# Performance work log

Measured on AMD Instinct MI355X. Metric: run time of the kernel, lower is better.

Reference implementation:

```python
import jax, jax.numpy as jnp
import numpy as np

SCALES = jnp.asarray([0.5, 1.0, 2.0], dtype=jnp.float32)  # distance_scales
GROUP_THRESHOLD = 2.0
EPS = 1e-6


def _pairwise_norm(x):
    # x: (B, T, N, 2) -> (B, T, N, N) euclidean distances, diagonal == 0
    diff = x[:, :, :, None, :] - x[:, :, None, :, :]
    sq = jnp.sum(diff * diff, axis=-1)
    safe = jnp.where(sq > 0, sq, 1.0)
    return jnp.where(sq > 0, jnp.sqrt(safe), 0.0)


def _assign_groups_one(d_last, threshold):
    # d_last: (N, N) pairwise distances at last timestep.
    # Sequential greedy grouping (faithful to the torch loop) via lax.scan over agents.
    N = d_last.shape[0]
    idx = jnp.arange(N)

    def step(carry, i):
        assigned, groups, cur = carry
        is_new = jnp.logical_not(assigned[i])  # agent i starts a new group
        # i itself (dist 0) plus unassigned j > i within threshold
        newly = is_new & jnp.logical_not(assigned) & (d_last[i] <= threshold) & (idx >= i)
        groups = jnp.where(newly, cur, groups)
        assigned = assigned | newly
        cur = cur + is_new.astype(jnp.int32)
        return (assigned, groups, cur), None

    init = (jnp.zeros(N, dtype=bool), jnp.zeros(N, dtype=jnp.int32), jnp.int32(0))
    (_, groups, _), _ = jax.lax.scan(step, init, idx)
    return groups


def setup_inputs() -> dict:
    key = jax.random.key(0)
    k1, k2 = jax.random.split(key)
    B, T, N = 8, 16, 256
    positions = jax.random.uniform(k1, (B, T, N, 2), dtype=jnp.float32) * 20.0
    displacements = jax.random.normal(k2, (B, T, N, 2), dtype=jnp.float32)
    return {"positions": positions, "displacements": displacements}


def reference(positions, displacements):
    # positions, displacements: (B, T, N, 2)
    pairwise_dist = _pairwise_norm(positions)       # (B, T, N, N)
    pairwise_disp = _pairwise_norm(displacements)   # (B, T, N, N)

    # build_relations: (B, R, T, N, N)
    dist_adj = (pairwise_dist[:, None] <= SCALES.reshape(1, -1, 1, 1, 1)).astype(pairwise_dist.dtype)
    disp_w = 1.0 / (pairwise_disp + EPS)
    disp_w = jnp.where(jnp.isinf(disp_w), 0.0, disp_w)
    adjacency = dist_adj * disp_w[:, None]

    # group assignment from last-timestep positions
    d_last = pairwise_dist[:, -1]  # (B, N, N)
    group_indices = jax.vmap(lambda d: _assign_groups_one(d, GROUP_THRESHOLD))(d_last)  # (B, N)

    # intra-group masking
    gmask = (group_indices[:, :, None] == group_indices[:, None, :]).astype(adjacency.dtype)  # (B, N, N)
    intra_adjacency = adjacency * gmask[:, None, None]

    return adjacency, group_indices, intra_adjacency
```

## Files before the change

### kernel.cpp

```cpp
#include <hip/hip_runtime.h>

#define NB 8
#define NT 16
#define NN 256
#define NS 3

typedef float f32x4 __attribute__((ext_vector_type(4)));
typedef int   i32x4 __attribute__((ext_vector_type(4)));

__global__ __launch_bounds__(64) void groups_kernel(
    const float* __restrict__ positions,
    float* __restrict__ out_groups_f,
    int* __restrict__ out_groups_i)
{
    const int b    = blockIdx.x;
    const int lane = threadIdx.x;

    const float2* __restrict__ P =
        ((const float2*)positions) + ((size_t)b * NT + (NT - 1)) * NN;

    float px[4], py[4];
#pragma unroll
    for (int k = 0; k < 4; ++k) {
        const float2 p = P[k * 64 + lane];
        px[k] = p.x; py[k] = p.y;
    }

    unsigned long long amask[4] = {0ull, 0ull, 0ull, 0ull};
    int grp[4] = {0, 0, 0, 0};
    int cur = 0;

#pragma unroll
    for (int ki = 0; ki < 4; ++ki) {
        for (int li = 0; li < 64; ++li) {
            if ((amask[ki] >> li) & 1ull) continue;
            const float pix = __shfl(px[ki], li);
            const float piy = __shfl(py[ki], li);
#pragma unroll
            for (int k = ki; k < 4; ++k) {
                const bool elig = (k > ki) || (lane >= li);
                const bool unas = (((amask[k] >> lane) & 1ull) == 0ull);
                const float dx = pix - px[k];
                const float dy = piy - py[k];
                const float sq = __fadd_rn(__fmul_rn(dx, dx), __fmul_rn(dy, dy));
                const float d  = (sq > 0.0f) ? __fsqrt_rn(sq) : 0.0f;
                const bool newly = elig && unas && (d <= 2.0f);
                const unsigned long long nb = __ballot(newly);
                amask[k] |= nb;
                if (newly) grp[k] = cur;
            }
            ++cur;
            if (!(~(amask[0] & amask[1] & amask[2] & amask[3]))) break;
        }
    }

#pragma unroll
    for (int k = 0; k < 4; ++k) {
        const int j = b * NN + k * 64 + lane;
        out_groups_i[j] = grp[k];
        out_groups_f[j] = (float)grp[k];
    }
}

#define PLANE_BLOCKS (NB * NS * NT * 2)

__global__ __launch_bounds__(256) void adj_kernel(
    const float* __restrict__ positions,
    const float* __restrict__ displacements,
    const int* __restrict__ groups,
    float* __restrict__ adj,
    float* __restrict__ intra)
{
    __shared__ float px[NN], py[NN], ux[NN], uy[NN];
    __shared__ int grp[NN];

    const int n       = blockIdx.x;
    const int isIntra = (n >= PLANE_BLOCKS) ? 1 : 0;
    const int slab    = isIntra ? (n - PLANE_BLOCKS) : n;
    const int half    = slab & 1;
    const int t       = (slab >> 1) & 15;
    const int bs      = slab >> 5;
    const int s       = bs % 3;
    const int b       = bs / 3;
    const int tid     = threadIdx.x;

    {
        const float2 p = ((const float2*)positions)[((size_t)b * NT + t) * NN + tid];
        const float2 u = ((const float2*)displacements)[((size_t)b * NT + t) * NN + tid];
        px[tid] = p.x;  py[tid] = p.y;
        ux[tid] = u.x;  uy[tid] = u.y;
        grp[tid] = groups[b * NN + tid];
    }
    __syncthreads();

    const int cl = tid & 63;
    const int rw = tid >> 6;

    const f32x4 pxj = ((const f32x4*)px)[cl];
    const f32x4 pyj = ((const f32x4*)py)[cl];
    const f32x4 uxj = ((const f32x4*)ux)[cl];
    const f32x4 uyj = ((const f32x4*)uy)[cl];
    const i32x4 gj  = ((const i32x4*)grp)[cl];

    const float S = (s == 0) ? 0.5f : ((s == 1) ? 1.0f : 2.0f);
    float* __restrict__ outp =
        (isIntra ? intra : adj) + ((size_t)bs * NT + t) * (size_t)(NN * NN);

    const int r0 = half * 128 + rw * 32;

    for (int q = 0; q < 32; ++q) {
        const int i = r0 + q;
        const float pix = px[i], piy = py[i];
        const float uix = ux[i], uiy = uy[i];
        const int   gi  = grp[i];

        f32x4 V;
#pragma unroll
        for (int cc = 0; cc < 4; ++cc) {
            const float dx = pix - pxj[cc];
            const float dy = piy - pyj[cc];
            const float sq = __fadd_rn(__fmul_rn(dx, dx), __fmul_rn(dy, dy));
            const float d  = __fsqrt_rn(sq);

            const float ex = uix - uxj[cc];
            const float ey = uiy - uyj[cc];
            const float sqe = __fadd_rn(__fmul_rn(ex, ex), __fmul_rn(ey, ey));
            const float dn  = __builtin_amdgcn_sqrtf(sqe);
            const float w   = __builtin_amdgcn_rcpf(dn + 1e-6f);

            const float gmv = (gi == gj[cc]) ? 1.0f : 0.0f;
            const float fac = isIntra ? gmv : 1.0f;
            V[cc] = (d <= S) ? w * fac : 0.0f;
        }

        *(f32x4*)(outp + (size_t)i * NN + 4 * cl) = V;
    }
}

extern "C" void kernel_launch(void* const* d_in, const int* in_sizes, int n_in,
                              void* d_out, int out_size, void* d_ws, size_t ws_size,
                              hipStream_t stream) {
    const float* positions     = (const float*)d_in[0];
    const float* displacements = (const float*)d_in[1];
    float* out = (float*)d_out;

    const size_t ADJ_ELEMS = (size_t)NB * NS * NT * NN * NN;
    float* adj      = out;
    float* groups_f = out + ADJ_ELEMS;
    float* intra    = out + ADJ_ELEMS + (size_t)NB * NN;
    int*   groups_i = (int*)d_ws;

    groups_kernel<<<NB, 64, 0, stream>>>(positions, groups_f, groups_i);
    adj_kernel<<<2 * PLANE_BLOCKS, 256, 0, stream>>>(positions, displacements,
                                                     groups_i, adj, intra);
}
```

Baseline: 220.9 us.

## Replace per-plane LDS blocks with persistent grid-stride wave sweep over output rows

The adjacency kernel now runs as a fixed grid of 1536 blocks in which each wave handles one output row per iteration. It reads the row's j-vectors straight from global memory, relying on cache, instead of staging them in shared memory behind a barrier. Writes go through a single output pointer that covers both the adjacency and the intra slabs. This removes the LDS staging and the per-block setup, and evens out the distribution of work. In exchange it repeats global loads of the position, displacement and group vectors for every row.

```diff
diff --git a/kernel.cpp b/kernel.cpp
--- a/kernel.cpp
+++ b/kernel.cpp
@@ -6,6 +6,7 @@
 #define NS 3
 
 typedef float f32x4 __attribute__((ext_vector_type(4)));
+typedef float f32x8 __attribute__((ext_vector_type(8)));
 typedef int   i32x4 __attribute__((ext_vector_type(4)));
 
 __global__ __launch_bounds__(64) void groups_kernel(
@@ -62,78 +63,67 @@
     }
 }
 
-#define PLANE_BLOCKS (NB * NS * NT * 2)
+#define TOTAL_CHUNKS (2 * NB * NS * NT * NN)
+#define SWEEP_BLOCKS 1536
+#define SWEEP_WAVES  (SWEEP_BLOCKS * 4)
+#define ITERS (TOTAL_CHUNKS / SWEEP_WAVES)
 
-__global__ __launch_bounds__(256) void adj_kernel(
+__global__ __launch_bounds__(256) void adj_sweep(
     const float* __restrict__ positions,
     const float* __restrict__ displacements,
-    const int* __restrict__ groups,
-    float* __restrict__ adj,
-    float* __restrict__ intra)
+    const int*   __restrict__ groups,
+    float* __restrict__ out)
 {
-    __shared__ float px[NN], py[NN], ux[NN], uy[NN];
-    __shared__ int grp[NN];
+    const int wid  = blockIdx.x * 4 + (threadIdx.x >> 6);
+    const int lane = threadIdx.x & 63;
 
-    const int n       = blockIdx.x;
-    const int isIntra = (n >= PLANE_BLOCKS) ? 1 : 0;
-    const int slab    = isIntra ? (n - PLANE_BLOCKS) : n;
-    const int half    = slab & 1;
-    const int t       = (slab >> 1) & 15;
-    const int bs      = slab >> 5;
-    const int s       = bs % 3;
-    const int b       = bs / 3;
-    const int tid     = threadIdx.x;
+    const size_t ADJ_F  = (size_t)NB * NS * NT * NN * NN;
+    const size_t INTRA0 = ADJ_F + (size_t)NB * NN;
 
-    {
-        const float2 p = ((const float2*)positions)[((size_t)b * NT + t) * NN + tid];
-        const float2 u = ((const float2*)displacements)[((size_t)b * NT + t) * NN + tid];
-        px[tid] = p.x;  py[tid] = p.y;
-        ux[tid] = u.x;  uy[tid] = u.y;
-        grp[tid] = groups[b * NN + tid];
-    }
-    __syncthreads();
+    for (int k = 0; k < ITERS; ++k) {
+        const int chunk = k * SWEEP_WAVES + wid;
+        const int isIn  = (chunk >= TOTAL_CHUNKS / 2) ? 1 : 0;
+        const int pc    = isIn ? (chunk - TOTAL_CHUNKS / 2) : chunk;
+        const int plane = pc >> 8;
+        const int i     = pc & 255;
+        const int t     = plane & 15;
+        const int bs    = plane >> 4;
+        const int s     = bs % 3;
+        const int b     = bs / 3;
+        const int pbase = (b * NT + t) * NN;
 
-    const int cl = tid & 63;
-    const int rw = tid >> 6;
+        const f32x8 pj = *(const f32x8*)(positions     + (size_t)(pbase + 4 * lane) * 2);
+        const f32x8 uj = *(const f32x8*)(displacements + (size_t)(pbase + 4 * lane) * 2);
+        const i32x4 gj = *(const i32x4*)(groups + b * NN + 4 * lane);
 
-    const f32x4 pxj = ((const f32x4*)px)[cl];
-    const f32x4 pyj = ((const f32x4*)py)[cl];
-    const f32x4 uxj = ((const f32x4*)ux)[cl];
-    const f32x4 uyj = ((const f32x4*)uy)[cl];
-    const i32x4 gj  = ((const i32x4*)grp)[cl];
+        const float2 pi = *(const float2*)(positions     + (size_t)(pbase + i) * 2);
+        const float2 ui = *(const float2*)(displacements + (size_t)(pbase + i) * 2);
+        const int    gi = groups[b * NN + i];
 
-    const float S = (s == 0) ? 0.5f : ((s == 1) ? 1.0f : 2.0f);
-    float* __restrict__ outp =
-        (isIntra ? intra : adj) + ((size_t)bs * NT + t) * (size_t)(NN * NN);
-
-    const int r0 = half * 128 + rw * 32;
-
-    for (int q = 0; q < 32; ++q) {
-        const int i = r0 + q;
-        const float pix = px[i], piy = py[i];
-        const float uix = ux[i], uiy = uy[i];
-        const int   gi  = grp[i];
+        const float S = (s == 0) ? 0.5f : ((s == 1) ? 1.0f : 2.0f);
 
         f32x4 V;
 #pragma unroll
         for (int cc = 0; cc < 4; ++cc) {
-            const float dx = pix - pxj[cc];
-            const float dy = piy - pyj[cc];
+            const float dx = pi.x - pj[2 * cc];
+            const float dy = pi.y - pj[2 * cc + 1];
             const float sq = __fadd_rn(__fmul_rn(dx, dx), __fmul_rn(dy, dy));
             const float d  = __fsqrt_rn(sq);
 
-            const float ex = uix - uxj[cc];
-            const float ey = uiy - uyj[cc];
+            const float ex = ui.x - uj[2 * cc];
+            const float ey = ui.y - uj[2 * cc + 1];
             const float sqe = __fadd_rn(__fmul_rn(ex, ex), __fmul_rn(ey, ey));
             const float dn  = __builtin_amdgcn_sqrtf(sqe);
             const float w   = __builtin_amdgcn_rcpf(dn + 1e-6f);
 
             const float gmv = (gi == gj[cc]) ? 1.0f : 0.0f;
-            const float fac = isIntra ? gmv : 1.0f;
+            const float fac = isIn ? gmv : 1.0f;
             V[cc] = (d <= S) ? w * fac : 0.0f;
         }
 
-        *(f32x4*)(outp + (size_t)i * NN + 4 * cl) = V;
+        const size_t dst = (isIn ? INTRA0 + (size_t)pc * NN
+                                 : (size_t)pc * NN) + 4 * lane;
+        *(f32x4*)(out + dst) = V;
     }
 }
 
@@ -145,12 +135,10 @@
     float* out = (float*)d_out;
 
     const size_t ADJ_ELEMS = (size_t)NB * NS * NT * NN * NN;
-    float* adj      = out;
     float* groups_f = out + ADJ_ELEMS;
-    float* intra    = out + ADJ_ELEMS + (size_t)NB * NN;
     int*   groups_i = (int*)d_ws;
 
     groups_kernel<<<NB, 64, 0, stream>>>(positions, groups_f, groups_i);
-    adj_kernel<<<2 * PLANE_BLOCKS, 256, 0, stream>>>(positions, displacements,
-                                                     groups_i, adj, intra);
+    adj_sweep<<<SWEEP_BLOCKS, 256, 0, stream>>>(positions, displacements,
+                                                groups_i, out);
 }
```

After: 246.5 us. 11.6% more time.
